# Kernel tuning notes

Measured on AMD Instinct MI355X. Metric: run time of the kernel, lower is better.

Reference implementation:

```python
import jax, jax.numpy as jnp
from jax import lax
import numpy as np

TOP_PERCENT = 1.3
KSIZE = 3
SIGMA = 0.3 * ((KSIZE - 1) * 0.5 - 1) + 0.8  # torchvision default sigma for ksize=3 -> 0.8


def _gaussian_kernel1d():
    x = jnp.arange(KSIZE, dtype=jnp.float32) - (KSIZE - 1) / 2.0
    k = jnp.exp(-0.5 * (x / SIGMA) ** 2)
    return k / k.sum()


def setup_inputs() -> dict:
    key = jax.random.key(0)
    img = jax.random.uniform(key, (3, 4096, 4096), dtype=jnp.float32)
    return {"img": img}


def reference(img):
    # --- rgb_to_grayscale (ITU-R 601 coefficients, as torchvision) ---
    gray = 0.2989 * img[0] + 0.587 * img[1] + 0.114 * img[2]  # [H, W]

    # --- separable 3x3 gaussian blur, reflect padding (torchvision) ---
    k = _gaussian_kernel1d()
    p = jnp.pad(gray, 1, mode="reflect")  # [H+2, W+2]
    # horizontal pass
    h = k[0] * p[:, :-2] + k[1] * p[:, 1:-1] + k[2] * p[:, 2:]  # [H+2, W]
    # vertical pass
    blur = k[0] * h[:-2, :] + k[1] * h[1:-1, :] + k[2] * h[2:, :]  # [H, W]

    # --- quantile threshold (linear interpolation, matches torch.quantile) ---
    q = (100.0 - TOP_PERCENT) / 100.0
    threshold = jnp.quantile(blur, q)
    mask = (blur >= threshold).astype(jnp.int32)  # [H, W]

    # --- binary opening with 5x5 ones footprint ---
    # erosion = min filter; outside-image treated as 0 (scipy border_value=0),
    # so pad explicitly with zeros and reduce with VALID windows.
    INT_MAX = np.iinfo(np.int32).max
    INT_MIN = np.iinfo(np.int32).min
    padded = jnp.pad(mask, 2)  # zero pad -> borders erode
    eroded = lax.reduce_window(padded, INT_MAX, lax.min, (5, 5), (1, 1), "VALID")
    # dilation = max filter; identity padding (-inf equiv) matches border_value=0
    opened = lax.reduce_window(eroded, INT_MIN, lax.max, (5, 5), (1, 1), "SAME")

    return opened[None, :, :].astype(jnp.int32)  # [1, H, W]
```

## Files before the change

kernel.cpp:

```cpp
#include <hip/hip_runtime.h>
#include <stdint.h>
#include <cmath>


#define HH 4096
#define WW 4096
#define KRANK 16559111u
#define CAP 65536u

__device__ __forceinline__ unsigned ukey(float v) {
  return (unsigned)(v * 268435456.0f);
}
__device__ __forceinline__ int refl(int i) {
  return i < 0 ? -i : (i > 4095 ? 8190 - i : i);
}
__device__ __forceinline__ float grayf(float r, float g, float b) {
  return __fadd_rn(__fadd_rn(__fmul_rn(0.2989f, r), __fmul_rn(0.587f, g)),
                   __fmul_rn(0.114f, b));
}
__device__ __forceinline__ float tap3(float a, float b, float c, float kn0, float kn1) {
  return __fadd_rn(__fadd_rn(__fmul_rn(kn0, a), __fmul_rn(kn1, b)),
                   __fmul_rn(kn0, c));
}

__global__ __launch_bounds__(512) void k_blur(const float* __restrict__ img,
    float4* __restrict__ blur4, unsigned* __restrict__ hist1,
    float kn0, float kn1) {
  __shared__ unsigned hist[4096];
  const int tid = threadIdx.x;
  #pragma unroll
  for (int i = tid; i < 4096; i += 512) hist[i] = 0u;
  __syncthreads();

  const int lane = tid & 63, wv = tid >> 6;
  const int bc = (blockIdx.x & 15) << 8;
  const int r0 = (blockIdx.x >> 4) << 6;
  const int rstart = r0 + (wv << 3);
  const float* __restrict__ Rp = img;
  const float* __restrict__ Gp = img + 16777216;
  const float* __restrict__ Bp = img + 33554432;
  const int c4 = bc + (lane << 2);
  const int colL = (bc == 0) ? 1 : bc - 1;
  const int colR = (bc == 3840) ? 4094 : bc + 256;
  const int hc = (lane == 0) ? colL : ((lane == 63) ? colR : c4);

  auto hrow = [&](int r) -> float4 {
    const size_t base = ((size_t)refl(r) << 12);
    float4 R = *(const float4*)(Rp + base + c4);
    float4 G = *(const float4*)(Gp + base + c4);
    float4 B = *(const float4*)(Bp + base + c4);
    float hr = Rp[base + hc], hg = Gp[base + hc], hb = Bp[base + hc];
    float4 g;
    g.x = grayf(R.x, G.x, B.x);
    g.y = grayf(R.y, G.y, B.y);
    g.z = grayf(R.z, G.z, B.z);
    g.w = grayf(R.w, G.w, B.w);
    float ghalo = grayf(hr, hg, hb);
    float gl = __shfl_up(g.w, 1);
    float gr_ = __shfl_down(g.x, 1);
    gl = (lane == 0) ? ghalo : gl;
    gr_ = (lane == 63) ? ghalo : gr_;
    float4 h;
    h.x = tap3(gl, g.x, g.y, kn0, kn1);
    h.y = tap3(g.x, g.y, g.z, kn0, kn1);
    h.z = tap3(g.y, g.z, g.w, kn0, kn1);
    h.w = tap3(g.z, g.w, gr_, kn0, kn1);
    return h;
  };

  float4 h0 = hrow(rstart - 1);
  float4 h1 = hrow(rstart);
  #pragma unroll
  for (int i = 0; i < 8; ++i) {
    float4 h2 = hrow(rstart + 1 + i);
    float4 v;
    v.x = tap3(h0.x, h1.x, h2.x, kn0, kn1);
    v.y = tap3(h0.y, h1.y, h2.y, kn0, kn1);
    v.z = tap3(h0.z, h1.z, h2.z, kn0, kn1);
    v.w = tap3(h0.w, h1.w, h2.w, kn0, kn1);
    blur4[(((size_t)(rstart + i) << 12) + c4) >> 2] = v;
    atomicAdd(&hist[ukey(v.x) >> 16], 1u);
    atomicAdd(&hist[ukey(v.y) >> 16], 1u);
    atomicAdd(&hist[ukey(v.z) >> 16], 1u);
    atomicAdd(&hist[ukey(v.w) >> 16], 1u);
    h0 = h1; h1 = h2;
  }
  __syncthreads();
  #pragma unroll
  for (int i = tid; i < 4096; i += 512) {
    unsigned c = hist[i];
    if (c) atomicAdd(&hist1[i], c);
  }
}

__global__ __launch_bounds__(256) void k_sel1(const unsigned* __restrict__ hist1,
                                              unsigned* __restrict__ sel) {
  __shared__ unsigned part[256];
  const int t = threadIdx.x;
  unsigned loc[16];
  unsigned s = 0;
  for (int i = 0; i < 16; ++i) { loc[i] = hist1[t * 16 + i]; s += loc[i]; }
  part[t] = s;
  __syncthreads();
  for (int off = 1; off < 256; off <<= 1) {
    unsigned v = (t >= off) ? part[t - off] : 0u;
    __syncthreads();
    part[t] += v;
    __syncthreads();
  }
  unsigned incl = part[t], excl = incl - s;
  if (excl <= KRANK && KRANK < incl) {
    unsigned p = excl;
    for (int i = 0; i < 16; ++i) {
      if (KRANK < p + loc[i]) { sel[0] = (unsigned)(t * 16 + i); sel[1] = KRANK - p; break; }
      p += loc[i];
    }
  }
}

__global__ __launch_bounds__(256) void k_pass2(const float* __restrict__ blur,
    const unsigned* __restrict__ sel, unsigned* __restrict__ hist2,
    unsigned* __restrict__ cnt, unsigned long long* __restrict__ list,
    unsigned long long* __restrict__ mbits) {
  __shared__ unsigned lcnt, lbase;
  __shared__ unsigned lidx[256];
  __shared__ unsigned short lkey[256];
  if (threadIdx.x == 0) lcnt = 0u;
  __syncthreads();
  const unsigned b1 = sel[0];
  const unsigned ub = (b1 + 1u) << 16;
  const unsigned base = blockIdx.x * 8192u + threadIdx.x;
  #pragma unroll 4
  for (int it = 0; it < 32; ++it) {
    unsigned i = base + (unsigned)it * 256u;
    unsigned u = ukey(blur[i]);
    unsigned long long w = __ballot(u >= ub);
    if ((threadIdx.x & 63) == 0) mbits[i >> 6] = w;
    if ((u >> 16) == b1) {
      atomicAdd(&hist2[u & 0xFFFFu], 1u);
      unsigned x = atomicAdd(&lcnt, 1u);
      if (x < 256u) { lidx[x] = i; lkey[x] = (unsigned short)(u & 0xFFFFu); }
      else {
        unsigned g = atomicAdd(cnt, 1u);
        if (g < CAP) list[g] = ((unsigned long long)i << 16) | (u & 0xFFFFu);
      }
    }
  }
  __syncthreads();
  unsigned n = lcnt > 256u ? 256u : lcnt;
  if (threadIdx.x == 0 && n) lbase = atomicAdd(cnt, n);
  __syncthreads();
  if (threadIdx.x < n) {
    unsigned g = lbase + threadIdx.x;
    if (g < CAP)
      list[g] = ((unsigned long long)lidx[threadIdx.x] << 16) | (unsigned)lkey[threadIdx.x];
  }
}

__global__ __launch_bounds__(1024) void k_sel2fix(const unsigned* __restrict__ hist2,
    const unsigned* __restrict__ sel, const unsigned* __restrict__ cnt,
    const unsigned long long* __restrict__ list,
    unsigned long long* __restrict__ mbits) {
  __shared__ unsigned part[1024];
  __shared__ unsigned sLo;
  const int t = threadIdx.x;
  const unsigned base = (unsigned)t * 64u;
  unsigned s = 0;
  for (int i = 0; i < 64; ++i) s += hist2[base + i];
  part[t] = s;
  __syncthreads();
  for (int off = 1; off < 1024; off <<= 1) {
    unsigned v = (t >= off) ? part[t - off] : 0u;
    __syncthreads();
    part[t] += v;
    __syncthreads();
  }
  unsigned incl = part[t], excl = incl - s;
  const unsigned r1 = sel[1];
  if (excl <= r1 && r1 < incl) {
    unsigned p = excl;
    for (int i = 0; i < 64; ++i) {
      unsigned c = hist2[base + i];
      if (r1 < p + c) { sLo = base + i; break; }
      p += c;
    }
  }
  __syncthreads();
  const unsigned lo = sLo;
  unsigned n = *cnt; if (n > CAP) n = CAP;
  for (unsigned j = t; j < n; j += 1024) {
    unsigned long long e = list[j];
    if ((unsigned)(e & 0xFFFFu) >= lo) {
      unsigned long long pix = e >> 16;
      atomicOr(&mbits[pix >> 6], 1ull << (pix & 63));
    }
  }
}

__global__ __launch_bounds__(256) void k_morph(
    const unsigned long long* __restrict__ mbits, int4* __restrict__ out4) {
  __shared__ unsigned long long er[12][64];
  __shared__ unsigned long long dl[8][64];
  const int r0 = blockIdx.x << 3;
  for (int t = threadIdx.x; t < 12 * 64; t += 256) {
    int lr = t >> 6, wc = t & 63;
    int rr = r0 - 2 + lr;
    unsigned long long acc = 0ull;
    if (rr >= 0 && rr < HH) {
      acc = ~0ull;
      #pragma unroll
      for (int dr = -2; dr <= 2; ++dr) {
        int mr = rr + dr;
        unsigned long long h = 0ull;
        if (mr >= 0 && mr < HH) {
          int rb = (mr << 6) + wc;
          unsigned long long C = mbits[rb];
          unsigned long long L = (wc > 0) ? mbits[rb - 1] : 0ull;
          unsigned long long R = (wc < 63) ? mbits[rb + 1] : 0ull;
          h = C & ((C >> 1) | (R << 63)) & ((C >> 2) | (R << 62))
                & ((C << 1) | (L >> 63)) & ((C << 2) | (L >> 62));
        }
        acc &= h;
      }
    }
    er[lr][wc] = acc;
  }
  __syncthreads();
  for (int t = threadIdx.x; t < 8 * 64; t += 256) {
    int lr = t >> 6, wc = t & 63;
    unsigned long long acc = 0ull;
    #pragma unroll
    for (int dr = 0; dr <= 4; ++dr) {
      unsigned long long C = er[lr + dr][wc];
      unsigned long long L = (wc > 0) ? er[lr + dr][wc - 1] : 0ull;
      unsigned long long R = (wc < 63) ? er[lr + dr][wc + 1] : 0ull;
      acc |= C | ((C >> 1) | (R << 63)) | ((C >> 2) | (R << 62))
               | ((C << 1) | (L >> 63)) | ((C << 2) | (L >> 62));
    }
    dl[lr][wc] = acc;
  }
  __syncthreads();
  const size_t p0 = (size_t)r0 << 10;
  for (int j = threadIdx.x; j < 8192; j += 256) {
    unsigned long long word = dl[j >> 10][(j >> 4) & 63];
    unsigned nib = (unsigned)(word >> ((j & 15) << 2)) & 0xFu;
    out4[p0 + j] = make_int4(nib & 1, (nib >> 1) & 1, (nib >> 2) & 1, (nib >> 3) & 1);
  }
}

extern "C" void kernel_launch(void* const* d_in, const int* in_sizes, int n_in,
                              void* d_out, int out_size, void* d_ws, size_t ws_size,
                              hipStream_t stream) {
  (void)in_sizes; (void)n_in; (void)out_size; (void)ws_size;
  const float* img = (const float*)d_in[0];
  char* ws = (char*)d_ws;

  float* blur = (float*)ws;
  unsigned* hist1 = (unsigned*)(ws + 67108864);
  unsigned* hist2 = (unsigned*)(ws + 67125248);
  unsigned* cnt   = (unsigned*)(ws + 67387392);
  unsigned* sel   = (unsigned*)(ws + 67387456);
  unsigned long long* list  = (unsigned long long*)(ws + 67387520);
  unsigned long long* mbits = (unsigned long long*)(ws + 67911808);

  float t = 1.0f / 0.8f;
  float k0 = expf(-0.5f * (t * t));
  float k1 = 1.0f;
  float s = (k0 + k1) + k0;
  float kn0 = k0 / s, kn1 = k1 / s;

  hipMemsetAsync(hist1, 0, 16384 + 262144 + 64, stream);
  k_blur<<<1024, 512, 0, stream>>>(img, (float4*)blur, hist1, kn0, kn1);
  k_sel1<<<1, 256, 0, stream>>>(hist1, sel);
  k_pass2<<<2048, 256, 0, stream>>>(blur, sel, hist2, cnt, list, mbits);
  k_sel2fix<<<1, 1024, 0, stream>>>(hist2, sel, cnt, list, mbits);
  k_morph<<<512, 256, 0, stream>>>(mbits, (int4*)d_out);
}
```

Before: 365.7 us.

## Prefetch blur rows, double rows per wave, replace global histogram atomics with partials

```diff
diff --git a/kernel.cpp b/kernel.cpp
--- a/kernel.cpp
+++ b/kernel.cpp
@@ -7,6 +7,7 @@
 #define WW 4096
 #define KRANK 16559111u
 #define CAP 65536u
+#define NBLK 512
 
 __device__ __forceinline__ unsigned ukey(float v) {
   return (unsigned)(v * 268435456.0f);
@@ -23,8 +24,10 @@
                    __fmul_rn(kn0, c));
 }
 
-__global__ __launch_bounds__(512) void k_blur(const float* __restrict__ img,
-    float4* __restrict__ blur4, unsigned* __restrict__ hist1,
+struct Raw { float4 R, G, B; float hr, hg, hb; };
+
+__global__ __launch_bounds__(512, 4) void k_blur(const float* __restrict__ img,
+    float4* __restrict__ blur4, unsigned* __restrict__ hist_part,
     float kn0, float kn1) {
   __shared__ unsigned hist[4096];
   const int tid = threadIdx.x;
@@ -34,8 +37,8 @@
 
   const int lane = tid & 63, wv = tid >> 6;
   const int bc = (blockIdx.x & 15) << 8;
-  const int r0 = (blockIdx.x >> 4) << 6;
-  const int rstart = r0 + (wv << 3);
+  const int r0 = (blockIdx.x >> 4) << 7;
+  const int rs = r0 + (wv << 4);
   const float* __restrict__ Rp = img;
   const float* __restrict__ Gp = img + 16777216;
   const float* __restrict__ Bp = img + 33554432;
@@ -44,18 +47,22 @@
   const int colR = (bc == 3840) ? 4094 : bc + 256;
   const int hc = (lane == 0) ? colL : ((lane == 63) ? colR : c4);
 
-  auto hrow = [&](int r) -> float4 {
+  auto ld = [&](int r) -> Raw {
+    Raw a;
     const size_t base = ((size_t)refl(r) << 12);
-    float4 R = *(const float4*)(Rp + base + c4);
-    float4 G = *(const float4*)(Gp + base + c4);
-    float4 B = *(const float4*)(Bp + base + c4);
-    float hr = Rp[base + hc], hg = Gp[base + hc], hb = Bp[base + hc];
+    a.R = *(const float4*)(Rp + base + c4);
+    a.G = *(const float4*)(Gp + base + c4);
+    a.B = *(const float4*)(Bp + base + c4);
+    a.hr = Rp[base + hc]; a.hg = Gp[base + hc]; a.hb = Bp[base + hc];
+    return a;
+  };
+  auto hcomp = [&](const Raw& a) -> float4 {
     float4 g;
-    g.x = grayf(R.x, G.x, B.x);
-    g.y = grayf(R.y, G.y, B.y);
-    g.z = grayf(R.z, G.z, B.z);
-    g.w = grayf(R.w, G.w, B.w);
-    float ghalo = grayf(hr, hg, hb);
+    g.x = grayf(a.R.x, a.G.x, a.B.x);
+    g.y = grayf(a.R.y, a.G.y, a.B.y);
+    g.z = grayf(a.R.z, a.G.z, a.B.z);
+    g.w = grayf(a.R.w, a.G.w, a.B.w);
+    float ghalo = grayf(a.hr, a.hg, a.hb);
     float gl = __shfl_up(g.w, 1);
     float gr_ = __shfl_down(g.x, 1);
     gl = (lane == 0) ? ghalo : gl;
@@ -68,29 +75,41 @@
     return h;
   };
 
-  float4 h0 = hrow(rstart - 1);
-  float4 h1 = hrow(rstart);
+  Raw A = ld(rs - 1);
+  Raw B = ld(rs);
+  float4 h0 = hcomp(A);
+  Raw C = ld(rs + 1);
+  float4 h1 = hcomp(B);
+  Raw D;
   #pragma unroll
-  for (int i = 0; i < 8; ++i) {
-    float4 h2 = hrow(rstart + 1 + i);
+  for (int i = 0; i < 16; ++i) {
+    if (i < 15) D = ld(rs + 2 + i);
+    float4 h2 = hcomp(C);
     float4 v;
     v.x = tap3(h0.x, h1.x, h2.x, kn0, kn1);
     v.y = tap3(h0.y, h1.y, h2.y, kn0, kn1);
     v.z = tap3(h0.z, h1.z, h2.z, kn0, kn1);
     v.w = tap3(h0.w, h1.w, h2.w, kn0, kn1);
-    blur4[(((size_t)(rstart + i) << 12) + c4) >> 2] = v;
+    blur4[(((size_t)(rs + i) << 12) + c4) >> 2] = v;
     atomicAdd(&hist[ukey(v.x) >> 16], 1u);
     atomicAdd(&hist[ukey(v.y) >> 16], 1u);
     atomicAdd(&hist[ukey(v.z) >> 16], 1u);
     atomicAdd(&hist[ukey(v.w) >> 16], 1u);
-    h0 = h1; h1 = h2;
-  }
-  __syncthreads();
+    h0 = h1; h1 = h2; C = D;
+  }
+  __syncthreads();
+  unsigned* dst = hist_part + (size_t)blockIdx.x * 4096;
   #pragma unroll
-  for (int i = tid; i < 4096; i += 512) {
-    unsigned c = hist[i];
-    if (c) atomicAdd(&hist1[i], c);
-  }
+  for (int i = tid; i < 4096; i += 512) dst[i] = hist[i];
+}
+
+__global__ __launch_bounds__(64) void k_hred(const unsigned* __restrict__ hp,
+                                             unsigned* __restrict__ hist1) {
+  const int t = blockIdx.x * 64 + threadIdx.x;
+  unsigned s = 0;
+  #pragma unroll 8
+  for (int k = 0; k < NBLK; ++k) s += hp[k * 4096 + t];
+  hist1[t] = s;
 }
 
 __global__ __launch_bounds__(256) void k_sel1(const unsigned* __restrict__ hist1,
@@ -164,9 +183,15 @@
   __shared__ unsigned part[1024];
   __shared__ unsigned sLo;
   const int t = threadIdx.x;
-  const unsigned base = (unsigned)t * 64u;
+  unsigned loc[64];
+  const uint4* h4 = (const uint4*)hist2;
   unsigned s = 0;
-  for (int i = 0; i < 64; ++i) s += hist2[base + i];
+  #pragma unroll
+  for (int j = 0; j < 16; ++j) {
+    uint4 q = h4[t * 16 + j];
+    loc[4 * j] = q.x; loc[4 * j + 1] = q.y; loc[4 * j + 2] = q.z; loc[4 * j + 3] = q.w;
+    s += q.x + q.y + q.z + q.w;
+  }
   part[t] = s;
   __syncthreads();
   for (int off = 1; off < 1024; off <<= 1) {
@@ -180,9 +205,8 @@
   if (excl <= r1 && r1 < incl) {
     unsigned p = excl;
     for (int i = 0; i < 64; ++i) {
-      unsigned c = hist2[base + i];
-      if (r1 < p + c) { sLo = base + i; break; }
-      p += c;
+      if (r1 < p + loc[i]) { sLo = (unsigned)t * 64u + i; break; }
+      p += loc[i];
     }
   }
   __syncthreads();
@@ -256,12 +280,13 @@
   char* ws = (char*)d_ws;
 
   float* blur = (float*)ws;
-  unsigned* hist1 = (unsigned*)(ws + 67108864);
-  unsigned* hist2 = (unsigned*)(ws + 67125248);
-  unsigned* cnt   = (unsigned*)(ws + 67387392);
-  unsigned* sel   = (unsigned*)(ws + 67387456);
-  unsigned long long* list  = (unsigned long long*)(ws + 67387520);
-  unsigned long long* mbits = (unsigned long long*)(ws + 67911808);
+  unsigned long long* mbits = (unsigned long long*)(ws + 67108864);
+  unsigned* hist_part = (unsigned*)(ws + 69206016);
+  unsigned* hist1 = (unsigned*)(ws + 77594624);
+  unsigned* hist2 = (unsigned*)(ws + 77611008);
+  unsigned* cnt   = (unsigned*)(ws + 77873152);
+  unsigned* sel   = (unsigned*)(ws + 77873216);
+  unsigned long long* list = (unsigned long long*)(ws + 77873280);
 
   float t = 1.0f / 0.8f;
   float k0 = expf(-0.5f * (t * t));
@@ -269,8 +294,9 @@
   float s = (k0 + k1) + k0;
   float kn0 = k0 / s, kn1 = k1 / s;
 
-  hipMemsetAsync(hist1, 0, 16384 + 262144 + 64, stream);
-  k_blur<<<1024, 512, 0, stream>>>(img, (float4*)blur, hist1, kn0, kn1);
+  hipMemsetAsync(hist2, 0, 262144 + 64, stream);
+  k_blur<<<512, 512, 0, stream>>>(img, (float4*)blur, hist_part, kn0, kn1);
+  k_hred<<<64, 64, 0, stream>>>(hist_part, hist1);
   k_sel1<<<1, 256, 0, stream>>>(hist1, sel);
   k_pass2<<<2048, 256, 0, stream>>>(blur, sel, hist2, cnt, list, mbits);
   k_sel2fix<<<1, 1024, 0, stream>>>(hist2, sel, cnt, list, mbits);
```

After: 378.4 us. 3.5% more time.
